# Kernel tuning notes

Measured on AMD Instinct MI355X. Metric: run time of the kernel, lower is better.

Reference implementation:

```python
import jax, jax.numpy as jnp
import numpy as np

B, N, D = 2, 2048, 2048
H, I, K, V = 16, 1, 128, 128
EPS = 1e-6


def setup_inputs() -> dict:
    key = jax.random.key(0)
    ks = jax.random.split(key, 6)
    x_q = jax.random.normal(ks[0], (B, N, D), dtype=jnp.float32)
    # norm_mask: lower-triangular causal mask (the 'nm' operand); values in [0,1]
    norm_mask = jnp.tril(jax.random.uniform(ks[1], (N, N), dtype=jnp.float32))
    scale = 1.0 / np.sqrt(D)
    w_q = jax.random.normal(ks[2], (D, H, I, K), dtype=jnp.float32) * scale
    w_k = jax.random.normal(ks[3], (D, H, K), dtype=jnp.float32) * scale
    w_v = jax.random.normal(ks[4], (D, H, V), dtype=jnp.float32) * scale
    w_o = jax.random.normal(ks[5], (H, I, V, D), dtype=jnp.float32) * (1.0 / np.sqrt(H * I * V))
    rms_scale = jnp.ones((V,), dtype=jnp.float32)
    return {"x_q": x_q, "norm_mask": norm_mask, "w_q": w_q, "w_k": w_k,
            "w_v": w_v, "rms_scale": rms_scale, "w_o": w_o}


def reference(x_q, norm_mask, w_q, w_k, w_v, rms_scale, w_o):
    # self-attention: x_k = x_v = x_q
    q = jnp.einsum('bnd,dhik->bnhik', x_q, w_q)   # (B,N,H,I,K)
    k = jnp.einsum('bnd,dhk->bnhk', x_q, w_k)     # (B,N,H,K)
    v = jnp.einsum('bnd,dhv->bnhv', x_q, w_v)     # (B,N,H,V)
    # linear (no-softmax) attention with decay/normalization mask 'nm'
    s = jnp.einsum('bnhik,bmhk->bnhim', q, k)     # (B,N,H,I,N)
    s = s * norm_mask[None, :, None, None, :]
    y = jnp.einsum('bnhim,bmhv->bnhiv', s, v)     # (B,N,H,I,V)
    # RMSNorm over v_head_d
    ms = jnp.mean(jnp.square(y), axis=-1, keepdims=True)
    y = y * jax.lax.rsqrt(ms + EPS) * rms_scale
    # output projection
    return jnp.einsum('bnhiv,hivd->bnd', y, w_o)
```

## Files before the change

kernel.cpp:

```cpp
#include <hip/hip_runtime.h>
#include <hip/hip_bf16.h>


typedef _Float16 f16x8 __attribute__((ext_vector_type(8)));
typedef _Float16 f16x4 __attribute__((ext_vector_type(4)));
typedef float    f32x4 __attribute__((ext_vector_type(4)));

#define DEV static __device__ __forceinline__

DEV int swzx(int row) { return (((row & 7) ^ ((row >> 3) & 7)) << 4); }

typedef const unsigned int __attribute__((address_space(1)))* gas_t;
typedef unsigned int __attribute__((address_space(3)))* las_t;
DEV void gld16(const void* g, void* l) {
  __builtin_amdgcn_global_load_lds((gas_t)g, (las_t)l, 16, 0, 0);
}

__global__ void k_cast_h(const float* __restrict__ in, _Float16* __restrict__ out, int n) {
  int i = (blockIdx.x * blockDim.x + threadIdx.x) * 4;
  int stride = gridDim.x * blockDim.x * 4;
  for (; i < n; i += stride) {
    float4 v = *reinterpret_cast<const float4*>(in + i);
    f16x4 o;
    o[0] = (_Float16)v.x; o[1] = (_Float16)v.y;
    o[2] = (_Float16)v.z; o[3] = (_Float16)v.w;
    *reinterpret_cast<f16x4*>(out + i) = o;
  }
}

__global__ void k_transpose_h4(const float* __restrict__ w0, const float* __restrict__ w1,
                               const float* __restrict__ w2, const float* __restrict__ w3,
                               _Float16* __restrict__ o0, _Float16* __restrict__ o1,
                               _Float16* __restrict__ o2, _Float16* __restrict__ o3) {
  __shared__ float tile[32][33];
  const float* in; _Float16* out;
  switch (blockIdx.z) {
    case 0: in = w0; out = o0; break;
    case 1: in = w1; out = o1; break;
    case 2: in = w2; out = o2; break;
    default: in = w3; out = o3; break;
  }
  int tx = threadIdx.x, ty = threadIdx.y;
  int c0 = blockIdx.x * 32, r0 = blockIdx.y * 32;
  #pragma unroll
  for (int j = 0; j < 4; ++j)
    tile[ty + j * 8][tx] = in[(size_t)(r0 + ty + j * 8) * 2048 + c0 + tx];
  __syncthreads();
  #pragma unroll
  for (int j = 0; j < 4; ++j)
    out[(size_t)(c0 + ty + j * 8) * 2048 + r0 + tx] = (_Float16)tile[tx][ty + j * 8];
}

__global__ void k_transpose_v(const _Float16* __restrict__ in, _Float16* __restrict__ out) {
  __shared__ _Float16 tile[32][33];
  int tx = threadIdx.x, ty = threadIdx.y;
  int v0 = blockIdx.x * 32, n0 = blockIdx.y * 32, bh = blockIdx.z;
  int b = bh >> 4, h = bh & 15;
  #pragma unroll
  for (int j = 0; j < 4; ++j)
    tile[ty + j * 8][tx] =
        in[(size_t)(b * 2048 + n0 + ty + j * 8) * 6144 + 4096 + h * 128 + v0 + tx];
  __syncthreads();
  #pragma unroll
  for (int j = 0; j < 4; ++j)
    out[((size_t)bh * 128 + v0 + ty + j * 8) * 2048 + n0 + tx] = tile[tx][ty + j * 8];
}

__global__ __launch_bounds__(512) void k_gemm256(const _Float16* __restrict__ A,
                                                 const _Float16* __restrict__ B,
                                                 _Float16* __restrict__ C, int ldc) {
  __shared__ __align__(16) _Float16 Ab[2][256 * 64];
  __shared__ __align__(16) _Float16 Bb[2][256 * 64];
  const int tid = threadIdx.x;
  const int lane = tid & 63, w = tid >> 6;
  const int lr = lane & 15, lg = lane >> 4;
  const int bm = blockIdx.y, bn = blockIdx.x;
  const int wr = (w >> 2) * 128, wc = (w & 3) * 64;

  f32x4 acc[8][4];
  #pragma unroll
  for (int i = 0; i < 8; ++i)
    #pragma unroll
    for (int j = 0; j < 4; ++j) { f32x4 z = {0.f, 0.f, 0.f, 0.f}; acc[i][j] = z; }

  const _Float16* aBase = A + (size_t)(bm * 256) * 2048;
  const _Float16* bBase = B + (size_t)(bn * 256) * 2048;

  const int srow = tid >> 3, sc8 = tid & 7;

  auto STAGE = [&](int kt, int bufi) {
    #pragma unroll
    for (int it = 0; it < 4; ++it) {
      int row = it * 64 + srow;
      int cb  = (sc8 * 16) ^ swzx(row);
      size_t g = (size_t)row * 2048 + kt * 64 + (cb >> 1);
      int ld = it * 8192 + tid * 16;
      gld16(aBase + g, (char*)Ab[bufi] + ld);
      gld16(bBase + g, (char*)Bb[bufi] + ld);
    }
  };

  STAGE(0, 0);
  asm volatile("s_waitcnt vmcnt(0)" ::: "memory");
  __builtin_amdgcn_s_barrier();
  __builtin_amdgcn_sched_barrier(0);

  for (int kt = 0; kt < 32; ++kt) {
    const int cur = kt & 1;
    if (kt + 1 < 32) STAGE(kt + 1, cur ^ 1);
    __builtin_amdgcn_sched_barrier(0);

    f16x8 bf[4];
    #pragma unroll
    for (int p = 0; p < 4; ++p) {
      const int ks = p >> 1, mh = p & 1;
      if (mh == 0) {
        #pragma unroll
        for (int nj = 0; nj < 4; ++nj) {
          int br = wc + nj * 16 + lr;
          bf[nj] = *reinterpret_cast<const f16x8*>(
              (const char*)Bb[cur] + br * 128 + ((ks * 64 + lg * 16) ^ swzx(br)));
        }
      }
      f16x8 af[4];
      #pragma unroll
      for (int m4 = 0; m4 < 4; ++m4) {
        int ar = wr + mh * 64 + m4 * 16 + lr;
        af[m4] = *reinterpret_cast<const f16x8*>(
            (const char*)Ab[cur] + ar * 128 + ((ks * 64 + lg * 16) ^ swzx(ar)));
      }
      __builtin_amdgcn_s_setprio(1);
      #pragma unroll
      for (int m4 = 0; m4 < 4; ++m4)
        #pragma unroll
        for (int nj = 0; nj < 4; ++nj)
          acc[mh * 4 + m4][nj] =
              __builtin_amdgcn_mfma_f32_16x16x32_f16(af[m4], bf[nj], acc[mh * 4 + m4][nj], 0, 0, 0);
      __builtin_amdgcn_s_setprio(0);
      __builtin_amdgcn_sched_barrier(0);
    }

    asm volatile("s_waitcnt vmcnt(0)" ::: "memory");
    __builtin_amdgcn_s_barrier();
    __builtin_amdgcn_sched_barrier(0);
  }

  #pragma unroll
  for (int mi = 0; mi < 8; ++mi)
    #pragma unroll
    for (int nj = 0; nj < 4; ++nj)
      #pragma unroll
      for (int r = 0; r < 4; ++r) {
        int grow = bm * 256 + wr + mi * 16 + lg * 4 + r;
        int gcol = bn * 256 + wc + nj * 16 + lr;
        C[(size_t)grow * ldc + gcol] = (_Float16)acc[mi][nj][r];
      }
}

__global__ __launch_bounds__(256) void k_gemm1(const _Float16* __restrict__ A,
                                               const _Float16* __restrict__ B,
                                               float* __restrict__ C, int ldc) {
  __shared__ __align__(16) _Float16 As[128 * 64];
  __shared__ __align__(16) _Float16 Bs[128 * 64];
  const int tid = threadIdx.x;
  const int lane = tid & 63, w = tid >> 6;
  const int lr = lane & 15, lg = lane >> 4;
  const int bm = blockIdx.y, bn = blockIdx.x;
  const int wr = (w >> 1) * 64, wc = (w & 1) * 64;

  f32x4 acc[4][4];
  #pragma unroll
  for (int i = 0; i < 4; ++i)
    #pragma unroll
    for (int j = 0; j < 4; ++j) { f32x4 z = {0.f, 0.f, 0.f, 0.f}; acc[i][j] = z; }

  const size_t aOff = (size_t)(bm * 128) * 2048;
  const size_t bOff = (size_t)(bn * 128) * 2048;

  for (int kt = 0; kt < 32; ++kt) {
    __syncthreads();
    #pragma unroll
    for (int it = 0; it < 4; ++it) {
      int row = it * 32 + (tid >> 3);
      int cb  = ((tid & 7) * 16) ^ swzx(row);
      size_t g = (size_t)row * 2048 + kt * 64 + (cb >> 1);
      int ld = it * 4096 + tid * 16;
      gld16(A + aOff + g, (char*)As + ld);
      gld16(B + bOff + g, (char*)Bs + ld);
    }
    __syncthreads();
    #pragma unroll
    for (int ks = 0; ks < 2; ++ks) {
      f16x8 af[4], bf[4];
      #pragma unroll
      for (int f = 0; f < 4; ++f) {
        int ar = wr + f * 16 + lr;
        af[f] = *reinterpret_cast<const f16x8*>((const char*)As + ar * 128 +
                                                ((ks * 64 + lg * 16) ^ swzx(ar)));
        int br = wc + f * 16 + lr;
        bf[f] = *reinterpret_cast<const f16x8*>((const char*)Bs + br * 128 +
                                                ((ks * 64 + lg * 16) ^ swzx(br)));
      }
      __builtin_amdgcn_s_setprio(1);
      #pragma unroll
      for (int i = 0; i < 4; ++i)
        #pragma unroll
        for (int j = 0; j < 4; ++j)
          acc[i][j] = __builtin_amdgcn_mfma_f32_16x16x32_f16(af[i], bf[j], acc[i][j], 0, 0, 0);
      __builtin_amdgcn_s_setprio(0);
    }
  }

  #pragma unroll
  for (int fm = 0; fm < 4; ++fm)
    #pragma unroll
    for (int fn = 0; fn < 4; ++fn)
      #pragma unroll
      for (int r = 0; r < 4; ++r) {
        int grow = bm * 128 + wr + fm * 16 + lg * 4 + r;
        int gcol = bn * 128 + wc + fn * 16 + lr;
        C[(size_t)grow * ldc + gcol] = acc[fm][fn][r];
      }
}

__global__ __launch_bounds__(256) void k_attn1(const _Float16* __restrict__ qkv,
                                               const _Float16* __restrict__ vt,
                                               const float* __restrict__ nm,
                                               const float* __restrict__ rms_scale,
                                               _Float16* __restrict__ y) {
  __shared__ __align__(16) _Float16 Ks[2][64 * 128];
  __shared__ __align__(16) _Float16 Vs[2][128 * 64];
  __shared__ __align__(16) _Float16 Ps[64 * 64];
  const int tid = threadIdx.x;
  const int lane = tid & 63, w = tid >> 6;
  const int lr = lane & 15, lg = lane >> 4;
  const int bh = blockIdx.x, b = bh >> 4, h = bh & 15;
  const _Float16* qb = qkv + (size_t)b * 2048 * 6144 + h * 128;
  const _Float16* kb = qkv + (size_t)b * 2048 * 6144 + 2048 + h * 128;
  const size_t vbase = (size_t)bh * 128 * 2048;

  const int krow = tid >> 4, kc = tid & 15;
  const int vrow = tid >> 3, vc = tid & 7;

  auto STAGE = [&](int t, int bufi) {
    #pragma unroll
    for (int it = 0; it < 4; ++it) {
      int kr = it * 16 + krow;
      int gk = ((kc * 16) ^ swzx(kr)) >> 1;
      gld16(kb + (size_t)(t * 64 + kr) * 6144 + gk,
            (char*)Ks[bufi] + it * 4096 + tid * 16);
      int vr = it * 32 + vrow;
      int gv = ((vc * 16) ^ swzx(vr)) >> 1;
      gld16(vt + vbase + (size_t)vr * 2048 + t * 64 + gv,
            (char*)Vs[bufi] + it * 4096 + tid * 16);
    }
  };

  #pragma unroll
  for (int pi = 0; pi < 2; ++pi) {
    const int qt = pi ? (31 - (int)blockIdx.y) : (int)blockIdx.y;
    const int nT = qt + 1;

    f16x8 aq[4];
    {
      const _Float16* qrow = qb + (size_t)(qt * 64 + w * 16 + lr) * 6144;
      #pragma unroll
      for (int ks = 0; ks < 4; ++ks)
        aq[ks] = *reinterpret_cast<const f16x8*>(qrow + ks * 32 + lg * 8);
    }

    f32x4 accY[8];
    #pragma unroll
    for (int i = 0; i < 8; ++i) { f32x4 z = {0.f, 0.f, 0.f, 0.f}; accY[i] = z; }

    STAGE(0, 0);
    asm volatile("s_waitcnt vmcnt(0)" ::: "memory");
    __builtin_amdgcn_s_barrier();
    __builtin_amdgcn_sched_barrier(0);

    for (int t = 0; t < nT; ++t) {
      const int cur = t & 1;

      float nmv[4][4];
      #pragma unroll
      for (int fm = 0; fm < 4; ++fm)
        #pragma unroll
        for (int r = 0; r < 4; ++r)
          nmv[fm][r] = nm[(size_t)(qt * 64 + w * 16 + lg * 4 + r) * 2048 +
                          t * 64 + fm * 16 + lr];
      __builtin_amdgcn_sched_barrier(0);

      if (t + 1 < nT) STAGE(t + 1, cur ^ 1);

      f32x4 accS[4];
      #pragma unroll
      for (int i = 0; i < 4; ++i) { f32x4 z = {0.f, 0.f, 0.f, 0.f}; accS[i] = z; }
      __builtin_amdgcn_s_setprio(1);
      #pragma unroll
      for (int ks = 0; ks < 4; ++ks) {
        #pragma unroll
        for (int fm = 0; fm < 4; ++fm) {
          int br = fm * 16 + lr;
          f16x8 bk = *reinterpret_cast<const f16x8*>(
              (const char*)Ks[cur] + br * 256 + ((ks * 64 + lg * 16) ^ swzx(br)));
          accS[fm] = __builtin_amdgcn_mfma_f32_16x16x32_f16(aq[ks], bk, accS[fm], 0, 0, 0);
        }
      }
      __builtin_amdgcn_s_setprio(0);

      #pragma unroll
      for (int fm = 0; fm < 4; ++fm)
        #pragma unroll
        for (int r = 0; r < 4; ++r) {
          float pv = accS[fm][r] * nmv[fm][r];
          int pr = w * 16 + lg * 4 + r, pc = fm * 16 + lr;
          *reinterpret_cast<_Float16*>((char*)Ps + pr * 128 + ((pc * 2) ^ swzx(pr))) =
              (_Float16)pv;
        }

      __builtin_amdgcn_s_setprio(1);
      #pragma unroll
      for (int ks = 0; ks < 2; ++ks) {
        int ar = w * 16 + lr;
        f16x8 ap = *reinterpret_cast<const f16x8*>(
            (const char*)Ps + ar * 128 + ((ks * 64 + lg * 16) ^ swzx(ar)));
        #pragma unroll
        for (int fv = 0; fv < 8; ++fv) {
          int br = fv * 16 + lr;
          f16x8 bv = *reinterpret_cast<const f16x8*>(
              (const char*)Vs[cur] + br * 128 + ((ks * 64 + lg * 16) ^ swzx(br)));
          accY[fv] = __builtin_amdgcn_mfma_f32_16x16x32_f16(ap, bv, accY[fv], 0, 0, 0);
        }
      }
      __builtin_amdgcn_s_setprio(0);

      asm volatile("s_waitcnt vmcnt(0)" ::: "memory");
      __builtin_amdgcn_s_barrier();
      __builtin_amdgcn_sched_barrier(0);
    }

    #pragma unroll
    for (int r = 0; r < 4; ++r) {
      float sq = 0.f;
      #pragma unroll
      for (int fv = 0; fv < 8; ++fv) { float yy = accY[fv][r]; sq += yy * yy; }
      sq += __shfl_xor(sq, 1); sq += __shfl_xor(sq, 2);
      sq += __shfl_xor(sq, 4); sq += __shfl_xor(sq, 8);
      float scale = rsqrtf(sq * (1.0f / 128.0f) + 1e-6f);
      int nrow = qt * 64 + w * 16 + lg * 4 + r;
      size_t orow = ((size_t)b * 2048 + nrow) * 2048 + (size_t)h * 128;
      #pragma unroll
      for (int fv = 0; fv < 8; ++fv) {
        int col = fv * 16 + lr;
        y[orow + col] = (_Float16)(accY[fv][r] * scale * rms_scale[col]);
      }
    }
  }
}

extern "C" void kernel_launch(void* const* d_in, const int* in_sizes, int n_in,
                              void* d_out, int out_size, void* d_ws, size_t ws_size,
                              hipStream_t stream) {
  (void)in_sizes; (void)n_in; (void)out_size; (void)ws_size;
  const float* x  = (const float*)d_in[0];
  const float* nm = (const float*)d_in[1];
  const float* wq = (const float*)d_in[2];
  const float* wk = (const float*)d_in[3];
  const float* wv = (const float*)d_in[4];
  const float* rs = (const float*)d_in[5];
  const float* wo = (const float*)d_in[6];

  _Float16* p = (_Float16*)d_ws;
  _Float16* xf  = p; p += 8388608;
  _Float16* wt3 = p; p += 12582912;
  _Float16* wto = p; p += 4194304;
  _Float16* qkv = p; p += 25165824;
  _Float16* vtf = p; p += 8388608;

  k_cast_h<<<dim3(2048), dim3(256), 0, stream>>>(x, xf, 8388608);

  k_transpose_h4<<<dim3(64, 64, 4), dim3(32, 8), 0, stream>>>(
      wq, wk, wv, wo, wt3, wt3 + 4194304, wt3 + 8388608, wto);

  k_gemm256<<<dim3(24, 16), dim3(512), 0, stream>>>(xf, wt3, qkv, 6144);
  k_transpose_v<<<dim3(4, 64, 32), dim3(32, 8), 0, stream>>>(qkv, vtf);

  k_attn1<<<dim3(32, 16), dim3(256), 0, stream>>>(qkv, vtf, nm, rs, xf);

  k_gemm1<<<dim3(16, 32), dim3(256), 0, stream>>>(xf, wto, (float*)d_out, 2048);
}
```

Baseline: 288.6 us.

## Stage GEMM tiles through registers with two-deep prefetch instead of direct-to-LDS loads

The 256x256 GEMM kernel stops using global_load_lds and instead loads tiles into registers two k-steps ahead, then writes them to LDS after each compute phase. The loop is unrolled by two with ping-pong register sets. Barriers are added around each MFMA phase so the waves run in lockstep, and launch bounds now request two blocks per CU. The aim is to hide global latency better, at the cost of extra register pressure, LDS store instructions and more barriers.

```diff
diff --git a/kernel.cpp b/kernel.cpp
--- a/kernel.cpp
+++ b/kernel.cpp
@@ -66,9 +66,9 @@
     out[((size_t)bh * 128 + v0 + ty + j * 8) * 2048 + n0 + tx] = tile[tx][ty + j * 8];
 }
 
-__global__ __launch_bounds__(512) void k_gemm256(const _Float16* __restrict__ A,
-                                                 const _Float16* __restrict__ B,
-                                                 _Float16* __restrict__ C, int ldc) {
+__global__ __launch_bounds__(512, 2) void k_gemm256(const _Float16* __restrict__ A,
+                                                    const _Float16* __restrict__ B,
+                                                    _Float16* __restrict__ C, int ldc) {
   __shared__ __align__(16) _Float16 Ab[2][256 * 64];
   __shared__ __align__(16) _Float16 Bb[2][256 * 64];
   const int tid = threadIdx.x;
@@ -88,28 +88,27 @@
 
   const int srow = tid >> 3, sc8 = tid & 7;
 
-  auto STAGE = [&](int kt, int bufi) {
+  f32x4 rA0[4], rB0[4], rA1[4], rB1[4];
+
+  auto ISSUE = [&](int kt, f32x4* ra, f32x4* rb) {
     #pragma unroll
     for (int it = 0; it < 4; ++it) {
       int row = it * 64 + srow;
       int cb  = (sc8 * 16) ^ swzx(row);
       size_t g = (size_t)row * 2048 + kt * 64 + (cb >> 1);
+      ra[it] = *reinterpret_cast<const f32x4*>(aBase + g);
+      rb[it] = *reinterpret_cast<const f32x4*>(bBase + g);
+    }
+  };
+  auto WRITE = [&](int c, const f32x4* ra, const f32x4* rb) {
+    #pragma unroll
+    for (int it = 0; it < 4; ++it) {
       int ld = it * 8192 + tid * 16;
-      gld16(aBase + g, (char*)Ab[bufi] + ld);
-      gld16(bBase + g, (char*)Bb[bufi] + ld);
+      *reinterpret_cast<f32x4*>((char*)Ab[c] + ld) = ra[it];
+      *reinterpret_cast<f32x4*>((char*)Bb[c] + ld) = rb[it];
     }
   };
-
-  STAGE(0, 0);
-  asm volatile("s_waitcnt vmcnt(0)" ::: "memory");
-  __builtin_amdgcn_s_barrier();
-  __builtin_amdgcn_sched_barrier(0);
-
-  for (int kt = 0; kt < 32; ++kt) {
-    const int cur = kt & 1;
-    if (kt + 1 < 32) STAGE(kt + 1, cur ^ 1);
-    __builtin_amdgcn_sched_barrier(0);
-
+  auto PHASES = [&](int c) {
     f16x8 bf[4];
     #pragma unroll
     for (int p = 0; p < 4; ++p) {
@@ -119,7 +118,7 @@
         for (int nj = 0; nj < 4; ++nj) {
           int br = wc + nj * 16 + lr;
           bf[nj] = *reinterpret_cast<const f16x8*>(
-              (const char*)Bb[cur] + br * 128 + ((ks * 64 + lg * 16) ^ swzx(br)));
+              (const char*)Bb[c] + br * 128 + ((ks * 64 + lg * 16) ^ swzx(br)));
         }
       }
       f16x8 af[4];
@@ -127,8 +126,9 @@
       for (int m4 = 0; m4 < 4; ++m4) {
         int ar = wr + mh * 64 + m4 * 16 + lr;
         af[m4] = *reinterpret_cast<const f16x8*>(
-            (const char*)Ab[cur] + ar * 128 + ((ks * 64 + lg * 16) ^ swzx(ar)));
-      }
+            (const char*)Ab[c] + ar * 128 + ((ks * 64 + lg * 16) ^ swzx(ar)));
+      }
+      __builtin_amdgcn_s_barrier();
       __builtin_amdgcn_s_setprio(1);
       #pragma unroll
       for (int m4 = 0; m4 < 4; ++m4)
@@ -137,12 +137,37 @@
           acc[mh * 4 + m4][nj] =
               __builtin_amdgcn_mfma_f32_16x16x32_f16(af[m4], bf[nj], acc[mh * 4 + m4][nj], 0, 0, 0);
       __builtin_amdgcn_s_setprio(0);
+      __builtin_amdgcn_s_barrier();
       __builtin_amdgcn_sched_barrier(0);
     }
-
-    asm volatile("s_waitcnt vmcnt(0)" ::: "memory");
+  };
+
+  ISSUE(0, rA0, rB0);
+  ISSUE(1, rA1, rB1);
+  __builtin_amdgcn_sched_barrier(0);
+  WRITE(0, rA0, rB0);
+  asm volatile("s_waitcnt lgkmcnt(0)" ::: "memory");
+  __builtin_amdgcn_s_barrier();
+  __builtin_amdgcn_sched_barrier(0);
+
+  for (int kt = 0; kt < 32; kt += 2) {
+    if (kt + 2 < 32) ISSUE(kt + 2, rA0, rB0);
+    __builtin_amdgcn_sched_barrier(0);
+    PHASES(0);
+    WRITE(1, rA1, rB1);
+    asm volatile("s_waitcnt lgkmcnt(0)" ::: "memory");
     __builtin_amdgcn_s_barrier();
     __builtin_amdgcn_sched_barrier(0);
+
+    if (kt + 3 < 32) ISSUE(kt + 3, rA1, rB1);
+    __builtin_amdgcn_sched_barrier(0);
+    PHASES(1);
+    if (kt + 2 < 32) {
+      WRITE(0, rA0, rB0);
+      asm volatile("s_waitcnt lgkmcnt(0)" ::: "memory");
+      __builtin_amdgcn_s_barrier();
+      __builtin_amdgcn_sched_barrier(0);
+    }
   }
 
   #pragma unroll
```

Result: slower. 684.4 us (+137.1%).

## Restructure QKV GEMM into 8-phase split-K pipeline and double-buffer output GEMM

Applied to the files above, without the earlier changes.

The QKV projection GEMM now stages each 64-wide K tile as two 32-wide halves in four LDS slices. Its schedule interleaves LDS fragment reads, next-tile global-to-LDS loads and MFMA bursts across eight barrier-separated phases, using partial vmcnt waits. Block indices are remapped so consecutive blocks spread across XCDs. The output projection GEMM gains LDS double buffering so global loads overlap MFMA work, in exchange for doubled LDS use and more barriers.

```diff
diff --git a/kernel.cpp b/kernel.cpp
--- a/kernel.cpp
+++ b/kernel.cpp
@@ -9,12 +9,18 @@
 #define DEV static __device__ __forceinline__
 
 DEV int swzx(int row) { return (((row & 7) ^ ((row >> 3) & 7)) << 4); }
+DEV int swz32(int row) { return (((row & 3) ^ ((row >> 2) & 3)) << 4); }
 
 typedef const unsigned int __attribute__((address_space(1)))* gas_t;
 typedef unsigned int __attribute__((address_space(3)))* las_t;
 DEV void gld16(const void* g, void* l) {
   __builtin_amdgcn_global_load_lds((gas_t)g, (las_t)l, 16, 0, 0);
 }
+
+#define SBAR()  __builtin_amdgcn_s_barrier()
+#define SCHED() __builtin_amdgcn_sched_barrier(0)
+#define LGKM0() asm volatile("s_waitcnt lgkmcnt(0)" ::: "memory")
+#define VM4()   asm volatile("s_waitcnt vmcnt(4)" ::: "memory")
 
 __global__ void k_cast_h(const float* __restrict__ in, _Float16* __restrict__ out, int n) {
   int i = (blockIdx.x * blockDim.x + threadIdx.x) * 4;
@@ -66,15 +72,16 @@
     out[((size_t)bh * 128 + v0 + ty + j * 8) * 2048 + n0 + tx] = tile[tx][ty + j * 8];
 }
 
-__global__ __launch_bounds__(512) void k_gemm256(const _Float16* __restrict__ A,
-                                                 const _Float16* __restrict__ B,
-                                                 _Float16* __restrict__ C, int ldc) {
-  __shared__ __align__(16) _Float16 Ab[2][256 * 64];
-  __shared__ __align__(16) _Float16 Bb[2][256 * 64];
+__global__ __launch_bounds__(512) void k_gemm8p(const _Float16* __restrict__ A,
+                                                const _Float16* __restrict__ B,
+                                                _Float16* __restrict__ C, int ldc) {
+  __shared__ __align__(16) _Float16 Asl[4][256 * 32];
+  __shared__ __align__(16) _Float16 Bsl[4][256 * 32];
   const int tid = threadIdx.x;
   const int lane = tid & 63, w = tid >> 6;
   const int lr = lane & 15, lg = lane >> 4;
-  const int bm = blockIdx.y, bn = blockIdx.x;
+  const int lid = ((int)blockIdx.x & 7) * 48 + ((int)blockIdx.x >> 3);
+  const int bm = lid / 24, bn = lid % 24;
   const int wr = (w >> 2) * 128, wc = (w & 3) * 64;
 
   f32x4 acc[8][4];
@@ -86,63 +93,80 @@
   const _Float16* aBase = A + (size_t)(bm * 256) * 2048;
   const _Float16* bBase = B + (size_t)(bn * 256) * 2048;
 
-  const int srow = tid >> 3, sc8 = tid & 7;
-
-  auto STAGE = [&](int kt, int bufi) {
-    #pragma unroll
-    for (int it = 0; it < 4; ++it) {
-      int row = it * 64 + srow;
-      int cb  = (sc8 * 16) ^ swzx(row);
-      size_t g = (size_t)row * 2048 + kt * 64 + (cb >> 1);
-      int ld = it * 8192 + tid * 16;
-      gld16(aBase + g, (char*)Ab[bufi] + ld);
-      gld16(bBase + g, (char*)Bb[bufi] + ld);
-    }
-  };
-
-  STAGE(0, 0);
-  asm volatile("s_waitcnt vmcnt(0)" ::: "memory");
-  __builtin_amdgcn_s_barrier();
-  __builtin_amdgcn_sched_barrier(0);
-
-  for (int kt = 0; kt < 32; ++kt) {
-    const int cur = kt & 1;
-    if (kt + 1 < 32) STAGE(kt + 1, cur ^ 1);
-    __builtin_amdgcn_sched_barrier(0);
-
-    f16x8 bf[4];
-    #pragma unroll
-    for (int p = 0; p < 4; ++p) {
-      const int ks = p >> 1, mh = p & 1;
-      if (mh == 0) {
-        #pragma unroll
-        for (int nj = 0; nj < 4; ++nj) {
-          int br = wc + nj * 16 + lr;
-          bf[nj] = *reinterpret_cast<const f16x8*>(
-              (const char*)Bb[cur] + br * 128 + ((ks * 64 + lg * 16) ^ swzx(br)));
-        }
-      }
-      f16x8 af[4];
-      #pragma unroll
-      for (int m4 = 0; m4 < 4; ++m4) {
-        int ar = wr + mh * 64 + m4 * 16 + lr;
-        af[m4] = *reinterpret_cast<const f16x8*>(
-            (const char*)Ab[cur] + ar * 128 + ((ks * 64 + lg * 16) ^ swzx(ar)));
-      }
-      __builtin_amdgcn_s_setprio(1);
-      #pragma unroll
-      for (int m4 = 0; m4 < 4; ++m4)
-        #pragma unroll
-        for (int nj = 0; nj < 4; ++nj)
-          acc[mh * 4 + m4][nj] =
-              __builtin_amdgcn_mfma_f32_16x16x32_f16(af[m4], bf[nj], acc[mh * 4 + m4][nj], 0, 0, 0);
-      __builtin_amdgcn_s_setprio(0);
-      __builtin_amdgcn_sched_barrier(0);
-    }
-
-    asm volatile("s_waitcnt vmcnt(0)" ::: "memory");
-    __builtin_amdgcn_s_barrier();
-    __builtin_amdgcn_sched_barrier(0);
+  const int s_cb = ((tid & 3) * 16) ^ (((((tid >> 2) & 3) ^ ((tid >> 4) & 3))) << 4);
+  const int swr = (((lr & 3) ^ ((lr >> 2) & 3)) << 4);
+
+  auto STAGE_A = [&](int T, int kh) {
+    #pragma unroll
+    for (int it = 0; it < 2; ++it) {
+      int row = it * 128 + (tid >> 2);
+      size_t g = (size_t)row * 2048 + T * 64 + kh * 32 + (s_cb >> 1);
+      gld16(aBase + g, (char*)Asl[(T & 1) * 2 + kh] + it * 8192 + tid * 16);
+    }
+  };
+  auto STAGE_B = [&](int T, int kh) {
+    #pragma unroll
+    for (int it = 0; it < 2; ++it) {
+      int row = it * 128 + (tid >> 2);
+      size_t g = (size_t)row * 2048 + T * 64 + kh * 32 + (s_cb >> 1);
+      gld16(bBase + g, (char*)Bsl[(T & 1) * 2 + kh] + it * 8192 + tid * 16);
+    }
+  };
+
+  f16x8 af[4], bf[4];
+  auto LOAD_B = [&](int d, int kh) {
+    #pragma unroll
+    for (int nj = 0; nj < 4; ++nj) {
+      int br = wc + nj * 16 + lr;
+      bf[nj] = *reinterpret_cast<const f16x8*>(
+          (const char*)Bsl[d * 2 + kh] + br * 64 + ((lg * 16) ^ swr));
+    }
+  };
+  auto LOAD_A = [&](int d, int kh, int mh) {
+    #pragma unroll
+    for (int m4 = 0; m4 < 4; ++m4) {
+      int ar = wr + mh * 64 + m4 * 16 + lr;
+      af[m4] = *reinterpret_cast<const f16x8*>(
+          (const char*)Asl[d * 2 + kh] + ar * 64 + ((lg * 16) ^ swr));
+    }
+  };
+  auto MFMA16 = [&](int mh) {
+    __builtin_amdgcn_s_setprio(1);
+    #pragma unroll
+    for (int m4 = 0; m4 < 4; ++m4)
+      #pragma unroll
+      for (int nj = 0; nj < 4; ++nj)
+        acc[mh * 4 + m4][nj] =
+            __builtin_amdgcn_mfma_f32_16x16x32_f16(af[m4], bf[nj], acc[mh * 4 + m4][nj], 0, 0, 0);
+    __builtin_amdgcn_s_setprio(0);
+  };
+
+  STAGE_A(0, 0); STAGE_B(0, 0); STAGE_A(0, 1); STAGE_B(0, 1);
+  VM4(); SCHED(); SBAR(); SCHED();
+
+  for (int T = 0; T < 32; ++T) {
+    const int d = T & 1;
+    const bool more = (T + 1 < 32);
+    LOAD_B(d, 0); LOAD_A(d, 0, 0);
+    if (more) STAGE_A(T + 1, 0);
+    SCHED(); SBAR(); LGKM0(); SCHED();
+    MFMA16(0);
+    SCHED(); SBAR(); SCHED();
+    LOAD_A(d, 0, 1);
+    if (more) STAGE_B(T + 1, 0);
+    SCHED(); SBAR(); LGKM0(); SCHED();
+    MFMA16(1);
+    VM4(); SCHED(); SBAR(); SCHED();
+    LOAD_B(d, 1); LOAD_A(d, 1, 0);
+    if (more) STAGE_A(T + 1, 1);
+    SCHED(); SBAR(); LGKM0(); SCHED();
+    MFMA16(0);
+    SCHED(); SBAR(); SCHED();
+    LOAD_A(d, 1, 1);
+    if (more) STAGE_B(T + 1, 1);
+    SCHED(); SBAR(); LGKM0(); SCHED();
+    MFMA16(1);
+    VM4(); SCHED(); SBAR(); SCHED();
   }
 
   #pragma unroll
@@ -151,17 +175,17 @@
     for (int nj = 0; nj < 4; ++nj)
       #pragma unroll
       for (int r = 0; r < 4; ++r) {
-        int grow = bm * 256 + wr + mi * 16 + lg * 4 + r;
+        int grow = bm * 256 + wr + (mi >> 2) * 64 + (mi & 3) * 16 + lg * 4 + r;
         int gcol = bn * 256 + wc + nj * 16 + lr;
         C[(size_t)grow * ldc + gcol] = (_Float16)acc[mi][nj][r];
       }
 }
 
-__global__ __launch_bounds__(256) void k_gemm1(const _Float16* __restrict__ A,
-                                               const _Float16* __restrict__ B,
-                                               float* __restrict__ C, int ldc) {
-  __shared__ __align__(16) _Float16 As[128 * 64];
-  __shared__ __align__(16) _Float16 Bs[128 * 64];
+__global__ __launch_bounds__(256) void k_gemm_db(const _Float16* __restrict__ A,
+                                                 const _Float16* __restrict__ B,
+                                                 float* __restrict__ C, int ldc) {
+  __shared__ __align__(16) _Float16 As[2][128 * 64];
+  __shared__ __align__(16) _Float16 Bs[2][128 * 64];
   const int tid = threadIdx.x;
   const int lane = tid & 63, w = tid >> 6;
   const int lr = lane & 15, lg = lane >> 4;
@@ -177,28 +201,36 @@
   const size_t aOff = (size_t)(bm * 128) * 2048;
   const size_t bOff = (size_t)(bn * 128) * 2048;
 
-  for (int kt = 0; kt < 32; ++kt) {
-    __syncthreads();
+  auto STAGE = [&](int kt, int bufi) {
     #pragma unroll
     for (int it = 0; it < 4; ++it) {
       int row = it * 32 + (tid >> 3);
       int cb  = ((tid & 7) * 16) ^ swzx(row);
       size_t g = (size_t)row * 2048 + kt * 64 + (cb >> 1);
       int ld = it * 4096 + tid * 16;
-      gld16(A + aOff + g, (char*)As + ld);
-      gld16(B + bOff + g, (char*)Bs + ld);
-    }
-    __syncthreads();
+      gld16(A + aOff + g, (char*)As[bufi] + ld);
+      gld16(B + bOff + g, (char*)Bs[bufi] + ld);
+    }
+  };
+
+  STAGE(0, 0);
+  asm volatile("s_waitcnt vmcnt(0)" ::: "memory");
+  SBAR(); SCHED();
+
+  for (int kt = 0; kt < 32; ++kt) {
+    const int cur = kt & 1;
+    if (kt + 1 < 32) STAGE(kt + 1, cur ^ 1);
+    SCHED();
     #pragma unroll
     for (int ks = 0; ks < 2; ++ks) {
       f16x8 af[4], bf[4];
       #pragma unroll
       for (int f = 0; f < 4; ++f) {
         int ar = wr + f * 16 + lr;
-        af[f] = *reinterpret_cast<const f16x8*>((const char*)As + ar * 128 +
+        af[f] = *reinterpret_cast<const f16x8*>((const char*)As[cur] + ar * 128 +
                                                 ((ks * 64 + lg * 16) ^ swzx(ar)));
         int br = wc + f * 16 + lr;
-        bf[f] = *reinterpret_cast<const f16x8*>((const char*)Bs + br * 128 +
+        bf[f] = *reinterpret_cast<const f16x8*>((const char*)Bs[cur] + br * 128 +
                                                 ((ks * 64 + lg * 16) ^ swzx(br)));
       }
       __builtin_amdgcn_s_setprio(1);
@@ -209,6 +241,8 @@
           acc[i][j] = __builtin_amdgcn_mfma_f32_16x16x32_f16(af[i], bf[j], acc[i][j], 0, 0, 0);
       __builtin_amdgcn_s_setprio(0);
     }
+    asm volatile("s_waitcnt vmcnt(0)" ::: "memory");
+    SBAR(); SCHED();
   }
 
   #pragma unroll
@@ -275,8 +309,7 @@
 
     STAGE(0, 0);
     asm volatile("s_waitcnt vmcnt(0)" ::: "memory");
-    __builtin_amdgcn_s_barrier();
-    __builtin_amdgcn_sched_barrier(0);
+    SBAR(); SCHED();
 
     for (int t = 0; t < nT; ++t) {
       const int cur = t & 1;
@@ -288,7 +321,7 @@
         for (int r = 0; r < 4; ++r)
           nmv[fm][r] = nm[(size_t)(qt * 64 + w * 16 + lg * 4 + r) * 2048 +
                           t * 64 + fm * 16 + lr];
-      __builtin_amdgcn_sched_barrier(0);
+      SCHED();
 
       if (t + 1 < nT) STAGE(t + 1, cur ^ 1);
 
@@ -335,8 +368,7 @@
       __builtin_amdgcn_s_setprio(0);
 
       asm volatile("s_waitcnt vmcnt(0)" ::: "memory");
-      __builtin_amdgcn_s_barrier();
-      __builtin_amdgcn_sched_barrier(0);
+      SBAR(); SCHED();
     }
 
     #pragma unroll
@@ -382,10 +414,10 @@
   k_transpose_h4<<<dim3(64, 64, 4), dim3(32, 8), 0, stream>>>(
       wq, wk, wv, wo, wt3, wt3 + 4194304, wt3 + 8388608, wto);
 
-  k_gemm256<<<dim3(24, 16), dim3(512), 0, stream>>>(xf, wt3, qkv, 6144);
+  k_gemm8p<<<dim3(384), dim3(512), 0, stream>>>(xf, wt3, qkv, 6144);
   k_transpose_v<<<dim3(4, 64, 32), dim3(32, 8), 0, stream>>>(qkv, vtf);
 
   k_attn1<<<dim3(32, 16), dim3(256), 0, stream>>>(qkv, vtf, nm, rs, xf);
 
-  k_gemm1<<<dim3(16, 32), dim3(256), 0, stream>>>(xf, wto, (float*)d_out, 2048);
-}
+  k_gemm_db<<<dim3(16, 32), dim3(256), 0, stream>>>(xf, wto, (float*)d_out, 2048);
+}
```

New measurement: 294.7 us. 1.02x slower.
